# Performance work log

Hardware: AMD Instinct MI355X
Metric: run time of the kernel (lower is better)

Reference implementation:

```python
import jax, jax.numpy as jnp
import numpy as np

G = 7          # 7x7 feature map -> 49 nodes per image
N = G * G
K = 3          # knn_k
NEG_SLOPE = 0.2  # PyG GATConv default leaky_relu slope


def build_spatial_edges():
    # 8-neighborhood grid edges on the 7x7 map, directed (src -> dst)
    src, dst = [], []
    for r in range(G):
        for c in range(G):
            i = r * G + c
            for dr in (-1, 0, 1):
                for dc in (-1, 0, 1):
                    if dr == 0 and dc == 0:
                        continue
                    rr, cc = r + dr, c + dc
                    if 0 <= rr < G and 0 <= cc < G:
                        src.append(rr * G + cc)
                        dst.append(i)
    return np.array([src, dst], dtype=np.int32)

SPATIAL = build_spatial_edges()  # [2, 312]


def build_edges(x):
    """x: [B, N, F] node features -> (src, dst) each [B, E].
    Edges = spatial 8-neighborhood + feature-space kNN (k=3) + self-loops."""
    B = x.shape[0]
    sq = jnp.sum(x * x, axis=-1)                               # [B, N]
    d = sq[:, :, None] + sq[:, None, :] - 2.0 * jnp.einsum('bnf,bmf->bnm', x, x)
    d = d + jnp.eye(N, dtype=x.dtype) * 1e9                    # exclude self
    _, nbr = jax.lax.top_k(-d, K)                              # [B, N, K]
    knn_src = nbr.reshape(B, N * K)
    knn_dst = jnp.broadcast_to(jnp.repeat(jnp.arange(N, dtype=jnp.int32), K)[None], (B, N * K))
    sp = jnp.asarray(SPATIAL)
    Es = sp.shape[1]
    loops = jnp.arange(N, dtype=jnp.int32)
    src = jnp.concatenate([jnp.broadcast_to(sp[0][None], (B, Es)), knn_src.astype(jnp.int32),
                           jnp.broadcast_to(loops[None], (B, N))], axis=1)
    dst = jnp.concatenate([jnp.broadcast_to(sp[1][None], (B, Es)), knn_dst,
                           jnp.broadcast_to(loops[None], (B, N))], axis=1)
    return src, dst


def gat_layer(x, src, dst, W, a_src, a_dst, b, concat):
    """PyG-style GATConv (eval mode, no dropout). x: [N,F], src/dst: [E]."""
    H, C = a_src.shape
    h = (x @ W).reshape(N, H, C)                               # [N, H, C]
    es = jnp.sum(h * a_src[None], axis=-1)                     # [N, H]
    ed = jnp.sum(h * a_dst[None], axis=-1)                     # [N, H]
    e = jax.nn.leaky_relu(es[src] + ed[dst], NEG_SLOPE)        # [E, H]
    m = jax.ops.segment_max(e, dst, num_segments=N)            # [N, H]
    m = jnp.where(jnp.isfinite(m), m, 0.0)
    p = jnp.exp(e - m[dst])
    denom = jax.ops.segment_sum(p, dst, num_segments=N)
    alpha = p / jnp.maximum(denom[dst], 1e-16)                 # softmax over incoming edges
    out = jax.ops.segment_sum(alpha[:, :, None] * h[src], dst, num_segments=N)  # [N, H, C]
    out = out.reshape(N, H * C) if concat else out.mean(axis=1)
    return out + b


def setup_inputs() -> dict:
    key = jax.random.key(0)
    ks = jax.random.split(key, 14)
    B, F, Hd, Cd, O, NC = 256, 1024, 8, 128, 256, 14
    s = 0.05
    return {
        'feat_map': jax.random.normal(ks[0], (B, F, G, G), dtype=jnp.float32),
        'W1': jax.random.normal(ks[1], (F, Hd * Cd), dtype=jnp.float32) * s,
        'a_src1': jax.random.normal(ks[2], (Hd, Cd), dtype=jnp.float32) * s,
        'a_dst1': jax.random.normal(ks[3], (Hd, Cd), dtype=jnp.float32) * s,
        'b1': jnp.zeros((Hd * Cd,), dtype=jnp.float32),
        'W2': jax.random.normal(ks[4], (Hd * Cd, O), dtype=jnp.float32) * s,
        'a_src2': jax.random.normal(ks[5], (1, O), dtype=jnp.float32) * s,
        'a_dst2': jax.random.normal(ks[6], (1, O), dtype=jnp.float32) * s,
        'b2': jnp.zeros((O,), dtype=jnp.float32),
        'Wc1': jax.random.normal(ks[7], (O, O), dtype=jnp.float32) * s,
        'bc1': jnp.zeros((O,), dtype=jnp.float32),
        'Wc2': jax.random.normal(ks[8], (O, NC), dtype=jnp.float32) * s,
        'bc2': jnp.zeros((NC,), dtype=jnp.float32),
    }


def reference(feat_map, W1, a_src1, a_dst1, b1, W2, a_src2, a_dst2, b2, Wc1, bc1, Wc2, bc2):
    B = feat_map.shape[0]
    # backbone output relu + flatten 7x7 map into 49 nodes
    x = jax.nn.relu(feat_map).reshape(B, -1, N).transpose(0, 2, 1)  # [B, N, 1024]
    src, dst = build_edges(x)

    def per_graph(xg, sg, dg):
        h = jax.nn.elu(gat_layer(xg, sg, dg, W1, a_src1, a_dst1, b1, True))
        h = jax.nn.elu(gat_layer(h, sg, dg, W2, a_src2, a_dst2, b2, False))
        return h.mean(axis=0)                                   # global mean pool -> [256]

    pooled = jax.vmap(per_graph)(x, src, dst)                   # [B, 256]
    return jax.nn.relu(pooled @ Wc1 + bc1) @ Wc2 + bc2          # [B, 14]
```

## Files before the change

kernel.cpp:

```cpp
#include <hip/hip_runtime.h>

#define GDIM 7
#define NN 49
#define FDIM 1024
#define HD 8
#define CD 128
#define ODIM 256
#define NC 14
#define MAXE 12

typedef __attribute__((ext_vector_type(4))) float f32x4;
typedef __attribute__((ext_vector_type(8))) short s16x8;

struct us4 { unsigned short x, y, z, w; };

__device__ __forceinline__ unsigned short f2bf(float x) {
  unsigned u = __float_as_uint(x);
  return (unsigned short)((u + 0x7fffu + ((u >> 16) & 1u)) >> 16);
}
__device__ __forceinline__ float bf2f(unsigned short h) {
  return __uint_as_float((unsigned)h << 16);
}

#define GLOAD_LDS16(g, l)                                          \
  __builtin_amdgcn_global_load_lds(                                \
      (const __attribute__((address_space(1))) void*)(g),          \
      (__attribute__((address_space(3))) void*)(l), 16, 0, 0)

__global__ void __launch_bounds__(256) relu_transpose_kernel(
    const float* __restrict__ F, float* __restrict__ X,
    unsigned short* __restrict__ Xh, unsigned short* __restrict__ Xl) {
  const int b  = blockIdx.x >> 4;
  const int f0 = (blockIdx.x & 15) << 6;
  const int tid = threadIdx.x;
  __shared__ float lds[64 * NN];
  const float* src = F + (size_t)b * FDIM * NN + (size_t)f0 * NN;
  for (int idx = tid; idx < 64 * NN; idx += 256) lds[idx] = src[idx];
  __syncthreads();
  for (int pass = 0; pass < 13; pass++) {
    int n = pass * 4 + (tid >> 6);
    int fi = tid & 63;
    if (n < NN) {
      float v = lds[fi * NN + n];
      v = v > 0.f ? v : 0.f;
      size_t o = ((size_t)b * NN + n) * FDIM + f0 + fi;
      X[o] = v;
      unsigned short h = f2bf(v);
      Xh[o] = h;
      Xl[o] = f2bf(v - bf2f(h));
    }
  }
}

__global__ void __launch_bounds__(256) knn_kernel(
    const float* __restrict__ X, int* __restrict__ knn) {
  const int b = blockIdx.x, tid = threadIdx.x;
  __shared__ float xs[56][68];
  __shared__ float gram[56][57];
  const float* Xb = X + (size_t)b * NN * FDIM;

  const int tr = tid / 14, tc = tid % 14;
  float acc[4][4];
#pragma unroll
  for (int i = 0; i < 4; i++)
#pragma unroll
    for (int j = 0; j < 4; j++) acc[i][j] = 0.f;

  for (int c0 = 0; c0 < FDIM; c0 += 64) {
    __syncthreads();
    for (int idx = tid; idx < NN * 16; idx += 256) {
      int n = idx >> 4, q = idx & 15;
      *(float4*)&xs[n][q << 2] =
          *(const float4*)&Xb[(size_t)n * FDIM + c0 + (q << 2)];
    }
    __syncthreads();
    if (tid < 196) {
#pragma unroll
      for (int k4 = 0; k4 < 64; k4 += 4) {
        float4 a[4], bb[4];
#pragma unroll
        for (int i = 0; i < 4; i++) a[i]  = *(const float4*)&xs[tr + 14 * i][k4];
#pragma unroll
        for (int j = 0; j < 4; j++) bb[j] = *(const float4*)&xs[tc + 14 * j][k4];
#pragma unroll
        for (int i = 0; i < 4; i++)
#pragma unroll
          for (int j = 0; j < 4; j++)
            acc[i][j] += a[i].x * bb[j].x + a[i].y * bb[j].y +
                         a[i].z * bb[j].z + a[i].w * bb[j].w;
      }
    }
  }
  if (tid < 196) {
#pragma unroll
    for (int i = 0; i < 4; i++)
#pragma unroll
      for (int j = 0; j < 4; j++) gram[tr + 14 * i][tc + 14 * j] = acc[i][j];
  }
  __syncthreads();
  if (tid < NN) {
    const int n = tid;
    const float sqn = gram[n][n];
    float d0 = 1e30f, d1 = 1e30f, d2 = 1e30f;
    int i0 = 0, i1 = 0, i2 = 0;
    for (int m = 0; m < NN; m++) {
      if (m == n) continue;
      float d = sqn + gram[m][m] - 2.f * gram[n][m];
      if (d < d0)      { d2=d1; i2=i1; d1=d0; i1=i0; d0=d; i0=m; }
      else if (d < d1) { d2=d1; i2=i1; d1=d;  i1=m; }
      else if (d < d2) { d2=d;  i2=m; }
    }
    knn[((size_t)b * NN + n) * 3 + 0] = i0;
    knn[((size_t)b * NN + n) * 3 + 1] = i1;
    knn[((size_t)b * NN + n) * 3 + 2] = i2;
  }
}

__global__ void __launch_bounds__(256) wconvT_kernel(
    const float* __restrict__ W, int K, int N,
    unsigned short* __restrict__ WhT, unsigned short* __restrict__ WlT) {
  __shared__ float t[64][65];
  const int nbx = N >> 6;
  const int bx = blockIdx.x % nbx, by = blockIdx.x / nbx;
  const int r0 = by << 6, c0 = bx << 6;
  const int tid = threadIdx.x;
#pragma unroll
  for (int i = 0; i < 16; i++) {
    int r = i * 4 + (tid >> 6), c = tid & 63;
    t[r][c] = W[(size_t)(r0 + r) * N + c0 + c];
  }
  __syncthreads();
#pragma unroll
  for (int i = 0; i < 16; i++) {
    int n = i * 4 + (tid >> 6);
    int k = tid & 63;
    float x = t[k][n];
    unsigned short h = f2bf(x);
    size_t o = (size_t)(c0 + n) * K + r0 + k;
    WhT[o] = h;
    WlT[o] = f2bf(x - bf2f(h));
  }
}

__global__ void __launch_bounds__(256) gemm_bf16x3(
    const unsigned short* __restrict__ A_h, const unsigned short* __restrict__ A_l,
    const unsigned short* __restrict__ BT_h, const unsigned short* __restrict__ BT_l,
    float* __restrict__ C, int M, int N, int K) {
  __shared__ unsigned short sAh[128][64], sAl[128][64];
  __shared__ unsigned short sBh[128][64], sBl[128][64];
  const int tid = threadIdx.x;
  const int w = tid >> 6, lane = tid & 63;
  const int nbx = N >> 7;
  const int nwg = gridDim.x;
  const int q = nwg >> 3, r = nwg & 7;
  const int xcd = blockIdx.x & 7, loc = blockIdx.x >> 3;
  const int wg = (xcd < r) ? (xcd * (q + 1) + loc)
                           : (r * (q + 1) + (xcd - r) * q + loc);
  const int bx = wg % nbx, by = wg / nbx;
  const int row0 = by << 7, col0 = bx << 7;
  const int wr = (w >> 1) << 6, wc = (w & 1) << 6;
  const int sgr = lane >> 3;
  const int schunk = lane & 7;
  const int fr = lane & 15;
  const int fq = lane >> 4;

  f32x4 acc[4][4];
#pragma unroll
  for (int m = 0; m < 4; m++)
#pragma unroll
    for (int n = 0; n < 4; n++) acc[m][n] = (f32x4){0.f, 0.f, 0.f, 0.f};

  for (int k0 = 0; k0 < K; k0 += 64) {
    __syncthreads();
#pragma unroll
    for (int i = 0; i < 4; i++) {
      const int rbase = (w << 5) + (i << 3);
      const int gr = rbase + sgr;
      const int sc = schunk ^ (gr & 7);
      const size_t ga = (size_t)(row0 + gr) * K + k0 + (sc << 3);
      GLOAD_LDS16(A_h + ga, &sAh[rbase][0]);
      GLOAD_LDS16(A_l + ga, &sAl[rbase][0]);
      const size_t gb = (size_t)(col0 + gr) * K + k0 + (sc << 3);
      GLOAD_LDS16(BT_h + gb, &sBh[rbase][0]);
      GLOAD_LDS16(BT_l + gb, &sBl[rbase][0]);
    }
    __syncthreads();
#pragma unroll
    for (int ks = 0; ks < 2; ks++) {
      const int cb = (ks << 2) + fq;
      s16x8 ah[4], al[4], bh[4], bl[4];
#pragma unroll
      for (int m = 0; m < 4; m++) {
        const int ra = wr + (m << 4) + fr;
        const int ca = (cb ^ (ra & 7)) << 3;
        ah[m] = *(const s16x8*)&sAh[ra][ca];
        al[m] = *(const s16x8*)&sAl[ra][ca];
        const int rb = wc + (m << 4) + fr;
        const int cbn = (cb ^ (rb & 7)) << 3;
        bh[m] = *(const s16x8*)&sBh[rb][cbn];
        bl[m] = *(const s16x8*)&sBl[rb][cbn];
      }
#pragma unroll
      for (int m = 0; m < 4; m++)
#pragma unroll
        for (int n = 0; n < 4; n++) {
          acc[m][n] = __builtin_amdgcn_mfma_f32_16x16x32_bf16(ah[m], bh[n], acc[m][n], 0, 0, 0);
          acc[m][n] = __builtin_amdgcn_mfma_f32_16x16x32_bf16(ah[m], bl[n], acc[m][n], 0, 0, 0);
          acc[m][n] = __builtin_amdgcn_mfma_f32_16x16x32_bf16(al[m], bh[n], acc[m][n], 0, 0, 0);
        }
    }
  }
  const int crow = fq << 2, ccol = fr;
#pragma unroll
  for (int m = 0; m < 4; m++)
#pragma unroll
    for (int n = 0; n < 4; n++)
#pragma unroll
      for (int v = 0; v < 4; v++)
        C[(size_t)(row0 + wr + (m << 4) + crow + v) * N + col0 + wc + (n << 4) + ccol] =
            acc[m][n][v];
}

__global__ void __launch_bounds__(256) attn1_prep(
    const float* __restrict__ H, const int* __restrict__ knn,
    const float* __restrict__ a_src, const float* __restrict__ a_dst,
    int* __restrict__ srcs_g, int* __restrict__ cnt_g,
    float* __restrict__ alpha_g) {
  const int b = blockIdx.x, tid = threadIdx.x;
  __shared__ float es[NN][HD], ed[NN][HD];
  __shared__ int srcs[NN][MAXE];
  __shared__ int cnt[NN];
  const float* Hb = H + (size_t)b * NN * FDIM;

  for (int p = tid; p < NN * HD; p += 256) {
    int n = p >> 3, h = p & 7;
    const float* hr = Hb + (size_t)n * FDIM + h * CD;
    float s1 = 0.f, s2 = 0.f;
    for (int c = 0; c < CD; c += 4) {
      float4 hv = *(const float4*)&hr[c];
      float4 as = *(const float4*)&a_src[h * CD + c];
      float4 ad = *(const float4*)&a_dst[h * CD + c];
      s1 += hv.x*as.x + hv.y*as.y + hv.z*as.z + hv.w*as.w;
      s2 += hv.x*ad.x + hv.y*ad.y + hv.z*ad.z + hv.w*ad.w;
    }
    es[n][h] = s1; ed[n][h] = s2;
  }
  if (tid < NN) {
    int i = tid, r = i / GDIM, c = i % GDIM, k = 0;
    for (int dr = -1; dr <= 1; dr++)
      for (int dc = -1; dc <= 1; dc++) {
        if (dr == 0 && dc == 0) continue;
        int rr = r + dr, cc = c + dc;
        if (rr >= 0 && rr < GDIM && cc >= 0 && cc < GDIM)
          srcs[i][k++] = rr * GDIM + cc;
      }
    srcs[i][k++] = knn[((size_t)b * NN + i) * 3 + 0];
    srcs[i][k++] = knn[((size_t)b * NN + i) * 3 + 1];
    srcs[i][k++] = knn[((size_t)b * NN + i) * 3 + 2];
    srcs[i][k++] = i;
    cnt[i] = k;
    cnt_g[(size_t)b * NN + i] = k;
    for (int j = 0; j < MAXE; j++)
      srcs_g[((size_t)b * NN + i) * MAXE + j] = srcs[i][j < k ? j : 0];
  }
  __syncthreads();
  for (int p = tid; p < NN * HD; p += 256) {
    int i = p >> 3, h = p & 7;
    int k = cnt[i];
    float e[MAXE];
    float m = -1e30f;
#pragma unroll
    for (int j = 0; j < MAXE; j++) {
      if (j < k) {
        float v = es[srcs[i][j]][h] + ed[i][h];
        v = v >= 0.f ? v : 0.2f * v;
        e[j] = v;
        m = fmaxf(m, v);
      }
    }
    float denom = 0.f;
#pragma unroll
    for (int j = 0; j < MAXE; j++) {
      if (j < k) { e[j] = expf(e[j] - m); denom += e[j]; }
    }
    float inv = 1.f / fmaxf(denom, 1e-16f);
#pragma unroll
    for (int j = 0; j < MAXE; j++) {
      if (j < k)
        alpha_g[(((size_t)b * NN + i) * MAXE + j) * HD + h] = e[j] * inv;
    }
  }
}

__global__ void __launch_bounds__(256) attn1_agg(
    const float* __restrict__ H, const int* __restrict__ srcs_g,
    const int* __restrict__ cnt_g, const float* __restrict__ alpha_g,
    const float* __restrict__ b1,
    unsigned short* __restrict__ Zh, unsigned short* __restrict__ Zl) {
  const int bid = blockIdx.x;
  const int b = bid / NN;
  const int tid = threadIdx.x;
  __shared__ float al[MAXE][HD];
  __shared__ int ss[MAXE];
  const int k = cnt_g[bid];
  if (tid < MAXE * HD) al[tid >> 3][tid & 7] = alpha_g[(size_t)bid * MAXE * HD + tid];
  if (tid < MAXE) ss[tid] = srcs_g[(size_t)bid * MAXE + tid];
  __syncthreads();
  const float4* Hb = (const float4*)(H + (size_t)b * NN * FDIM);
  const int h = tid >> 5;
  float4 acc = ((const float4*)b1)[tid];
  for (int j = 0; j < k; j++) {
    float a = al[j][h];
    float4 v = Hb[(size_t)ss[j] * (FDIM / 4) + tid];
    acc.x += a * v.x; acc.y += a * v.y; acc.z += a * v.z; acc.w += a * v.w;
  }
  acc.x = acc.x > 0.f ? acc.x : expm1f(acc.x);
  acc.y = acc.y > 0.f ? acc.y : expm1f(acc.y);
  acc.z = acc.z > 0.f ? acc.z : expm1f(acc.z);
  acc.w = acc.w > 0.f ? acc.w : expm1f(acc.w);
  us4 hv, lv;
  hv.x = f2bf(acc.x); lv.x = f2bf(acc.x - bf2f(hv.x));
  hv.y = f2bf(acc.y); lv.y = f2bf(acc.y - bf2f(hv.y));
  hv.z = f2bf(acc.z); lv.z = f2bf(acc.z - bf2f(hv.z));
  hv.w = f2bf(acc.w); lv.w = f2bf(acc.w - bf2f(hv.w));
  *(us4*)&Zh[(size_t)bid * FDIM + (tid << 2)] = hv;
  *(us4*)&Zl[(size_t)bid * FDIM + (tid << 2)] = lv;
}

__global__ void __launch_bounds__(256) attn2_prep(
    const float* __restrict__ H2, const int* __restrict__ srcs_g,
    const int* __restrict__ cnt_g, const float* __restrict__ a_src,
    const float* __restrict__ a_dst, float* __restrict__ alpha_g) {
  const int b = blockIdx.x, tid = threadIdx.x;
  __shared__ float es[NN], ed[NN];
  const float* Hb = H2 + (size_t)b * NN * ODIM;
  if (tid < NN) {
    const float* hr = Hb + (size_t)tid * ODIM;
    float s1 = 0.f, s2 = 0.f;
    for (int c = 0; c < ODIM; c += 4) {
      float4 hv = *(const float4*)&hr[c];
      float4 as = *(const float4*)&a_src[c];
      float4 ad = *(const float4*)&a_dst[c];
      s1 += hv.x*as.x + hv.y*as.y + hv.z*as.z + hv.w*as.w;
      s2 += hv.x*ad.x + hv.y*ad.y + hv.z*ad.z + hv.w*ad.w;
    }
    es[tid] = s1; ed[tid] = s2;
  }
  __syncthreads();
  if (tid < NN) {
    const int i = tid;
    const int k = cnt_g[(size_t)b * NN + i];
    float e[MAXE];
    float m = -1e30f;
#pragma unroll
    for (int j = 0; j < MAXE; j++) {
      if (j < k) {
        int s = srcs_g[((size_t)b * NN + i) * MAXE + j];
        float v = es[s] + ed[i];
        v = v >= 0.f ? v : 0.2f * v;
        e[j] = v;
        m = fmaxf(m, v);
      }
    }
    float denom = 0.f;
#pragma unroll
    for (int j = 0; j < MAXE; j++) {
      if (j < k) { e[j] = expf(e[j] - m); denom += e[j]; }
    }
    float inv = 1.f / fmaxf(denom, 1e-16f);
#pragma unroll
    for (int j = 0; j < MAXE; j++) {
      if (j < k) alpha_g[((size_t)b * NN + i) * MAXE + j] = e[j] * inv;
    }
  }
}

__global__ void __launch_bounds__(256) attn2_agg(
    const float* __restrict__ H2, const int* __restrict__ srcs_g,
    const int* __restrict__ cnt_g, const float* __restrict__ alpha_g,
    const float* __restrict__ b2, float* __restrict__ Z2) {
  const int bid = blockIdx.x;
  const int b = bid / NN;
  const int tid = threadIdx.x;
  __shared__ float al[MAXE];
  __shared__ int ss[MAXE];
  const int k = cnt_g[bid];
  if (tid < MAXE) {
    al[tid] = alpha_g[(size_t)bid * MAXE + tid];
    ss[tid] = srcs_g[(size_t)bid * MAXE + tid];
  }
  __syncthreads();
  const float* Hb = H2 + (size_t)b * NN * ODIM;
  float acc = b2[tid];
  for (int j = 0; j < k; j++)
    acc += al[j] * Hb[(size_t)ss[j] * ODIM + tid];
  acc = acc > 0.f ? acc : expm1f(acc);
  Z2[(size_t)bid * ODIM + tid] = acc;
}

__global__ void __launch_bounds__(256) pool_kernel(
    const float* __restrict__ Z2, float* __restrict__ pooled) {
  const int b = blockIdx.x, c = threadIdx.x;
  float s = 0.f;
  for (int i = 0; i < NN; i++)
    s += Z2[((size_t)b * NN + i) * ODIM + c];
  pooled[(size_t)b * ODIM + c] = s * (1.f / 49.f);
}

__global__ void __launch_bounds__(256) classifier_kernel(
    const float* __restrict__ pooled, const float* __restrict__ Wc1,
    const float* __restrict__ bc1, const float* __restrict__ Wc2,
    const float* __restrict__ bc2, float* __restrict__ out) {
  const int b = blockIdx.x, tid = threadIdx.x;
  __shared__ float p[ODIM];
  __shared__ float t[ODIM];
  p[tid] = pooled[(size_t)b * ODIM + tid];
  __syncthreads();
  float a = bc1[tid];
  for (int c = 0; c < ODIM; c++) a += p[c] * Wc1[(size_t)c * ODIM + tid];
  t[tid] = a > 0.f ? a : 0.f;
  __syncthreads();
  if (tid < NC) {
    float o = bc2[tid];
    for (int j = 0; j < ODIM; j++) o += t[j] * Wc2[(size_t)j * NC + tid];
    out[(size_t)b * NC + tid] = o;
  }
}

extern "C" void kernel_launch(void* const* d_in, const int* in_sizes, int n_in,
                              void* d_out, int out_size, void* d_ws, size_t ws_size,
                              hipStream_t stream) {
  const float* feat   = (const float*)d_in[0];
  const float* W1     = (const float*)d_in[1];
  const float* a_src1 = (const float*)d_in[2];
  const float* a_dst1 = (const float*)d_in[3];
  const float* b1     = (const float*)d_in[4];
  const float* W2     = (const float*)d_in[5];
  const float* a_src2 = (const float*)d_in[6];
  const float* a_dst2 = (const float*)d_in[7];
  const float* b2     = (const float*)d_in[8];
  const float* Wc1    = (const float*)d_in[9];
  const float* bc1    = (const float*)d_in[10];
  const float* Wc2    = (const float*)d_in[11];
  const float* bc2    = (const float*)d_in[12];

  const int B = in_sizes[0] / (FDIM * NN);
  const int M = B * NN;

  const size_t xE = (size_t)M * FDIM;
  float* X  = (float*)d_ws;
  float* H1 = X + xE;
  unsigned short* Xh = (unsigned short*)(H1 + xE);
  unsigned short* Xl = Xh + xE;
  unsigned short* W1hT = Xl + xE;
  unsigned short* W1lT = W1hT + (size_t)FDIM * FDIM;
  unsigned short* W2hT = W1lT + (size_t)FDIM * FDIM;
  unsigned short* W2lT = W2hT + (size_t)ODIM * FDIM;
  int*   knn    = (int*)(W2lT + (size_t)ODIM * FDIM);
  int*   srcs_g = knn + (size_t)M * 3;
  int*   cnt_g  = srcs_g + (size_t)M * MAXE;
  float* alpha1 = (float*)(cnt_g + M);
  float* alpha2 = alpha1 + (size_t)M * MAXE * HD;
  float* pooled = alpha2 + (size_t)M * MAXE;
  float* H2  = X;
  float* Z2  = H1;
  unsigned short* Z1h = Xh;
  unsigned short* Z1l = Xl;

  relu_transpose_kernel<<<B * 16, 256, 0, stream>>>(feat, X, Xh, Xl);
  knn_kernel<<<B, 256, 0, stream>>>(X, knn);
  wconvT_kernel<<<(FDIM / 64) * (FDIM / 64), 256, 0, stream>>>(W1, FDIM, FDIM, W1hT, W1lT);
  wconvT_kernel<<<(FDIM / 64) * (ODIM / 64), 256, 0, stream>>>(W2, FDIM, ODIM, W2hT, W2lT);
  gemm_bf16x3<<<(M / 128) * (FDIM / 128), 256, 0, stream>>>(
      Xh, Xl, W1hT, W1lT, H1, M, FDIM, FDIM);
  attn1_prep<<<B, 256, 0, stream>>>(H1, knn, a_src1, a_dst1, srcs_g, cnt_g, alpha1);
  attn1_agg<<<M, 256, 0, stream>>>(H1, srcs_g, cnt_g, alpha1, b1, Z1h, Z1l);
  gemm_bf16x3<<<(M / 128) * (ODIM / 128), 256, 0, stream>>>(
      Z1h, Z1l, W2hT, W2lT, H2, M, ODIM, FDIM);
  attn2_prep<<<B, 256, 0, stream>>>(H2, srcs_g, cnt_g, a_src2, a_dst2, alpha2);
  attn2_agg<<<M, 256, 0, stream>>>(H2, srcs_g, cnt_g, alpha2, b2, Z2);
  pool_kernel<<<B, 256, 0, stream>>>(Z2, pooled);
  classifier_kernel<<<B, 256, 0, stream>>>(pooled, Wc1, bc1, Wc2, bc2, (float*)d_out);
}
```

Measured before the change: 325.2 us.

## Split kNN gram and attention score kernels across more blocks; fuse pooling

```diff
diff --git a/kernel.cpp b/kernel.cpp
--- a/kernel.cpp
+++ b/kernel.cpp
@@ -8,6 +8,8 @@
 #define ODIM 256
 #define NC 14
 #define MAXE 12
+#define KSPLIT 4
+#define GPSTRIDE 3192
 
 typedef __attribute__((ext_vector_type(4))) float f32x4;
 typedef __attribute__((ext_vector_type(8))) short s16x8;
@@ -52,12 +54,13 @@
   }
 }
 
-__global__ void __launch_bounds__(256) knn_kernel(
-    const float* __restrict__ X, int* __restrict__ knn) {
-  const int b = blockIdx.x, tid = threadIdx.x;
+__global__ void __launch_bounds__(256) knn_partial(
+    const float* __restrict__ X, float* __restrict__ gramP) {
+  const int gid = blockIdx.x;
+  const int b = gid >> 2, p = gid & 3;
+  const int tid = threadIdx.x;
   __shared__ float xs[56][68];
-  __shared__ float gram[56][57];
-  const float* Xb = X + (size_t)b * NN * FDIM;
+  const float* Xb = X + (size_t)b * NN * FDIM + p * 256;
 
   const int tr = tid / 14, tc = tid % 14;
   float acc[4][4];
@@ -66,7 +69,7 @@
 #pragma unroll
     for (int j = 0; j < 4; j++) acc[i][j] = 0.f;
 
-  for (int c0 = 0; c0 < FDIM; c0 += 64) {
+  for (int c0 = 0; c0 < 256; c0 += 64) {
     __syncthreads();
     for (int idx = tid; idx < NN * 16; idx += 256) {
       int n = idx >> 4, q = idx & 15;
@@ -92,10 +95,25 @@
     }
   }
   if (tid < 196) {
+    float* gp = gramP + (size_t)gid * GPSTRIDE;
 #pragma unroll
     for (int i = 0; i < 4; i++)
 #pragma unroll
-      for (int j = 0; j < 4; j++) gram[tr + 14 * i][tc + 14 * j] = acc[i][j];
+      for (int j = 0; j < 4; j++)
+        gp[(tr + 14 * i) * 57 + tc + 14 * j] = acc[i][j];
+  }
+}
+
+__global__ void __launch_bounds__(256) knn_select(
+    const float* __restrict__ gramP, int* __restrict__ knn) {
+  const int b = blockIdx.x, tid = threadIdx.x;
+  __shared__ float gram[NN][50];
+  const float* g0 = gramP + (size_t)(b * KSPLIT) * GPSTRIDE;
+  for (int idx = tid; idx < NN * NN; idx += 256) {
+    int r = idx / NN, c = idx % NN;
+    float s = g0[r * 57 + c] + g0[GPSTRIDE + r * 57 + c] +
+              g0[2 * GPSTRIDE + r * 57 + c] + g0[3 * GPSTRIDE + r * 57 + c];
+    gram[r][c] = s;
   }
   __syncthreads();
   if (tid < NN) {
@@ -221,29 +239,44 @@
             acc[m][n][v];
 }
 
-__global__ void __launch_bounds__(256) attn1_prep(
-    const float* __restrict__ H, const int* __restrict__ knn,
-    const float* __restrict__ a_src, const float* __restrict__ a_dst,
-    int* __restrict__ srcs_g, int* __restrict__ cnt_g,
-    float* __restrict__ alpha_g) {
+__global__ void __launch_bounds__(256) esed1_kernel(
+    const float* __restrict__ H, const float* __restrict__ a_src,
+    const float* __restrict__ a_dst, float* __restrict__ es_g,
+    float* __restrict__ ed_g) {
+  const int n = blockIdx.x * 4 + (threadIdx.x >> 6);
+  const int lane = threadIdx.x & 63;
+  const int h = lane >> 3, sub = lane & 7;
+  const float* hr = H + (size_t)n * FDIM + h * CD + sub * 16;
+  const float* as = a_src + h * CD + sub * 16;
+  const float* ad = a_dst + h * CD + sub * 16;
+  float s1 = 0.f, s2 = 0.f;
+#pragma unroll
+  for (int c = 0; c < 16; c += 4) {
+    float4 hv = *(const float4*)&hr[c];
+    float4 av = *(const float4*)&as[c];
+    float4 dv = *(const float4*)&ad[c];
+    s1 += hv.x*av.x + hv.y*av.y + hv.z*av.z + hv.w*av.w;
+    s2 += hv.x*dv.x + hv.y*dv.y + hv.z*dv.z + hv.w*dv.w;
+  }
+  s1 += __shfl_xor(s1, 1); s1 += __shfl_xor(s1, 2); s1 += __shfl_xor(s1, 4);
+  s2 += __shfl_xor(s2, 1); s2 += __shfl_xor(s2, 2); s2 += __shfl_xor(s2, 4);
+  if (sub == 0) {
+    es_g[(size_t)n * HD + h] = s1;
+    ed_g[(size_t)n * HD + h] = s2;
+  }
+}
+
+__global__ void __launch_bounds__(256) attn1_soft(
+    const float* __restrict__ es_g, const float* __restrict__ ed_g,
+    const int* __restrict__ knn, int* __restrict__ srcs_g,
+    int* __restrict__ cnt_g, float* __restrict__ alpha_g) {
   const int b = blockIdx.x, tid = threadIdx.x;
   __shared__ float es[NN][HD], ed[NN][HD];
   __shared__ int srcs[NN][MAXE];
   __shared__ int cnt[NN];
-  const float* Hb = H + (size_t)b * NN * FDIM;
-
   for (int p = tid; p < NN * HD; p += 256) {
-    int n = p >> 3, h = p & 7;
-    const float* hr = Hb + (size_t)n * FDIM + h * CD;
-    float s1 = 0.f, s2 = 0.f;
-    for (int c = 0; c < CD; c += 4) {
-      float4 hv = *(const float4*)&hr[c];
-      float4 as = *(const float4*)&a_src[h * CD + c];
-      float4 ad = *(const float4*)&a_dst[h * CD + c];
-      s1 += hv.x*as.x + hv.y*as.y + hv.z*as.z + hv.w*as.w;
-      s2 += hv.x*ad.x + hv.y*ad.y + hv.z*ad.z + hv.w*ad.w;
-    }
-    es[n][h] = s1; ed[n][h] = s2;
+    es[p >> 3][p & 7] = es_g[(size_t)b * NN * HD + p];
+    ed[p >> 3][p & 7] = ed_g[(size_t)b * NN * HD + p];
   }
   if (tid < NN) {
     int i = tid, r = i / GDIM, c = i % GDIM, k = 0;
@@ -327,24 +360,34 @@
   *(us4*)&Zl[(size_t)bid * FDIM + (tid << 2)] = lv;
 }
 
-__global__ void __launch_bounds__(256) attn2_prep(
-    const float* __restrict__ H2, const int* __restrict__ srcs_g,
-    const int* __restrict__ cnt_g, const float* __restrict__ a_src,
-    const float* __restrict__ a_dst, float* __restrict__ alpha_g) {
+__global__ void __launch_bounds__(256) esed2_kernel(
+    const float* __restrict__ H2, const float* __restrict__ a_src,
+    const float* __restrict__ a_dst, float* __restrict__ es_g,
+    float* __restrict__ ed_g) {
+  const int n = blockIdx.x * 4 + (threadIdx.x >> 6);
+  const int lane = threadIdx.x & 63;
+  float4 hv = *(const float4*)&H2[(size_t)n * ODIM + lane * 4];
+  float4 av = *(const float4*)&a_src[lane * 4];
+  float4 dv = *(const float4*)&a_dst[lane * 4];
+  float s1 = hv.x*av.x + hv.y*av.y + hv.z*av.z + hv.w*av.w;
+  float s2 = hv.x*dv.x + hv.y*dv.y + hv.z*dv.z + hv.w*dv.w;
+#pragma unroll
+  for (int m = 1; m < 64; m <<= 1) {
+    s1 += __shfl_xor(s1, m);
+    s2 += __shfl_xor(s2, m);
+  }
+  if (lane == 0) { es_g[n] = s1; ed_g[n] = s2; }
+}
+
+__global__ void __launch_bounds__(256) attn2_soft(
+    const float* __restrict__ es_g, const float* __restrict__ ed_g,
+    const int* __restrict__ srcs_g, const int* __restrict__ cnt_g,
+    float* __restrict__ alpha_g) {
   const int b = blockIdx.x, tid = threadIdx.x;
   __shared__ float es[NN], ed[NN];
-  const float* Hb = H2 + (size_t)b * NN * ODIM;
   if (tid < NN) {
-    const float* hr = Hb + (size_t)tid * ODIM;
-    float s1 = 0.f, s2 = 0.f;
-    for (int c = 0; c < ODIM; c += 4) {
-      float4 hv = *(const float4*)&hr[c];
-      float4 as = *(const float4*)&a_src[c];
-      float4 ad = *(const float4*)&a_dst[c];
-      s1 += hv.x*as.x + hv.y*as.y + hv.z*as.z + hv.w*as.w;
-      s2 += hv.x*ad.x + hv.y*ad.y + hv.z*ad.z + hv.w*ad.w;
-    }
-    es[tid] = s1; ed[tid] = s2;
+    es[tid] = es_g[(size_t)b * NN + tid];
+    ed[tid] = ed_g[(size_t)b * NN + tid];
   }
   __syncthreads();
   if (tid < NN) {
@@ -398,23 +441,17 @@
   Z2[(size_t)bid * ODIM + tid] = acc;
 }
 
-__global__ void __launch_bounds__(256) pool_kernel(
-    const float* __restrict__ Z2, float* __restrict__ pooled) {
-  const int b = blockIdx.x, c = threadIdx.x;
-  float s = 0.f;
-  for (int i = 0; i < NN; i++)
-    s += Z2[((size_t)b * NN + i) * ODIM + c];
-  pooled[(size_t)b * ODIM + c] = s * (1.f / 49.f);
-}
-
 __global__ void __launch_bounds__(256) classifier_kernel(
-    const float* __restrict__ pooled, const float* __restrict__ Wc1,
+    const float* __restrict__ Z2, const float* __restrict__ Wc1,
     const float* __restrict__ bc1, const float* __restrict__ Wc2,
     const float* __restrict__ bc2, float* __restrict__ out) {
   const int b = blockIdx.x, tid = threadIdx.x;
   __shared__ float p[ODIM];
   __shared__ float t[ODIM];
-  p[tid] = pooled[(size_t)b * ODIM + tid];
+  float s = 0.f;
+  for (int i = 0; i < NN; i++)
+    s += Z2[((size_t)b * NN + i) * ODIM + tid];
+  p[tid] = s * (1.f / 49.f);
   __syncthreads();
   float a = bc1[tid];
   for (int c = 0; c < ODIM; c++) a += p[c] * Wc1[(size_t)c * ODIM + tid];
@@ -461,24 +498,30 @@
   int*   cnt_g  = srcs_g + (size_t)M * MAXE;
   float* alpha1 = (float*)(cnt_g + M);
   float* alpha2 = alpha1 + (size_t)M * MAXE * HD;
-  float* pooled = alpha2 + (size_t)M * MAXE;
+  float* gramP  = alpha2 + (size_t)M * MAXE;
+  float* es1    = gramP + (size_t)B * KSPLIT * GPSTRIDE;
+  float* ed1    = es1 + (size_t)M * HD;
+  float* es2    = ed1 + (size_t)M * HD;
+  float* ed2    = es2 + M;
   float* H2  = X;
   float* Z2  = H1;
   unsigned short* Z1h = Xh;
   unsigned short* Z1l = Xl;
 
   relu_transpose_kernel<<<B * 16, 256, 0, stream>>>(feat, X, Xh, Xl);
-  knn_kernel<<<B, 256, 0, stream>>>(X, knn);
+  knn_partial<<<B * KSPLIT, 256, 0, stream>>>(X, gramP);
+  knn_select<<<B, 256, 0, stream>>>(gramP, knn);
   wconvT_kernel<<<(FDIM / 64) * (FDIM / 64), 256, 0, stream>>>(W1, FDIM, FDIM, W1hT, W1lT);
   wconvT_kernel<<<(FDIM / 64) * (ODIM / 64), 256, 0, stream>>>(W2, FDIM, ODIM, W2hT, W2lT);
   gemm_bf16x3<<<(M / 128) * (FDIM / 128), 256, 0, stream>>>(
       Xh, Xl, W1hT, W1lT, H1, M, FDIM, FDIM);
-  attn1_prep<<<B, 256, 0, stream>>>(H1, knn, a_src1, a_dst1, srcs_g, cnt_g, alpha1);
+  esed1_kernel<<<M / 4, 256, 0, stream>>>(H1, a_src1, a_dst1, es1, ed1);
+  attn1_soft<<<B, 256, 0, stream>>>(es1, ed1, knn, srcs_g, cnt_g, alpha1);
   attn1_agg<<<M, 256, 0, stream>>>(H1, srcs_g, cnt_g, alpha1, b1, Z1h, Z1l);
   gemm_bf16x3<<<(M / 128) * (ODIM / 128), 256, 0, stream>>>(
       Z1h, Z1l, W2hT, W2lT, H2, M, ODIM, FDIM);
-  attn2_prep<<<B, 256, 0, stream>>>(H2, srcs_g, cnt_g, a_src2, a_dst2, alpha2);
+  esed2_kernel<<<M / 4, 256, 0, stream>>>(H2, a_src2, a_dst2, es2, ed2);
+  attn2_soft<<<B, 256, 0, stream>>>(es2, ed2, srcs_g, cnt_g, alpha2);
   attn2_agg<<<M, 256, 0, stream>>>(H2, srcs_g, cnt_g, alpha2, b2, Z2);
-  pool_kernel<<<B, 256, 0, stream>>>(Z2, pooled);
-  classifier_kernel<<<B, 256, 0, stream>>>(pooled, Wc1, bc1, Wc2, bc2, (float*)d_out);
-}
+  classifier_kernel<<<B, 256, 0, stream>>>(Z2, Wc1, bc1, Wc2, bc2, (float*)d_out);
+}
```

Result: no change. 328.9 us (+1.2%).

## Fuse attention logits into GEMM epilogues and drop prep and pool kernels

Applied to the files above, without the earlier changes.

```diff
diff --git a/kernel.cpp b/kernel.cpp
--- a/kernel.cpp
+++ b/kernel.cpp
@@ -53,7 +53,8 @@
 }
 
 __global__ void __launch_bounds__(256) knn_kernel(
-    const float* __restrict__ X, int* __restrict__ knn) {
+    const float* __restrict__ X, int* __restrict__ srcs_g,
+    int* __restrict__ cnt_g) {
   const int b = blockIdx.x, tid = threadIdx.x;
   __shared__ float xs[56][68];
   __shared__ float gram[56][57];
@@ -110,9 +111,20 @@
       else if (d < d1) { d2=d1; i2=i1; d1=d;  i1=m; }
       else if (d < d2) { d2=d;  i2=m; }
     }
-    knn[((size_t)b * NN + n) * 3 + 0] = i0;
-    knn[((size_t)b * NN + n) * 3 + 1] = i1;
-    knn[((size_t)b * NN + n) * 3 + 2] = i2;
+    int srcs[MAXE];
+    int r = n / GDIM, c = n % GDIM, k = 0;
+    for (int dr = -1; dr <= 1; dr++)
+      for (int dc = -1; dc <= 1; dc++) {
+        if (dr == 0 && dc == 0) continue;
+        int rr = r + dr, cc = c + dc;
+        if (rr >= 0 && rr < GDIM && cc >= 0 && cc < GDIM)
+          srcs[k++] = rr * GDIM + cc;
+      }
+    srcs[k++] = i0; srcs[k++] = i1; srcs[k++] = i2;
+    srcs[k++] = n;
+    cnt_g[(size_t)b * NN + n] = k;
+    for (int j = 0; j < MAXE; j++)
+      srcs_g[((size_t)b * NN + n) * MAXE + j] = srcs[j < k ? j : 0];
   }
 }
 
@@ -145,7 +157,9 @@
 __global__ void __launch_bounds__(256) gemm_bf16x3(
     const unsigned short* __restrict__ A_h, const unsigned short* __restrict__ A_l,
     const unsigned short* __restrict__ BT_h, const unsigned short* __restrict__ BT_l,
-    float* __restrict__ C, int M, int N, int K) {
+    float* __restrict__ C, int M, int N, int K,
+    const float* __restrict__ av, const float* __restrict__ dv,
+    float* __restrict__ esp, float* __restrict__ edp) {
   __shared__ unsigned short sAh[128][64], sAl[128][64];
   __shared__ unsigned short sBh[128][64], sBl[128][64];
   const int tid = threadIdx.x;
@@ -219,92 +233,86 @@
       for (int v = 0; v < 4; v++)
         C[(size_t)(row0 + wr + (m << 4) + crow + v) * N + col0 + wc + (n << 4) + ccol] =
             acc[m][n][v];
-}
-
-__global__ void __launch_bounds__(256) attn1_prep(
-    const float* __restrict__ H, const int* __restrict__ knn,
-    const float* __restrict__ a_src, const float* __restrict__ a_dst,
-    int* __restrict__ srcs_g, int* __restrict__ cnt_g,
-    float* __restrict__ alpha_g) {
-  const int b = blockIdx.x, tid = threadIdx.x;
-  __shared__ float es[NN][HD], ed[NN][HD];
-  __shared__ int srcs[NN][MAXE];
-  __shared__ int cnt[NN];
-  const float* Hb = H + (size_t)b * NN * FDIM;
-
-  for (int p = tid; p < NN * HD; p += 256) {
-    int n = p >> 3, h = p & 7;
-    const float* hr = Hb + (size_t)n * FDIM + h * CD;
-    float s1 = 0.f, s2 = 0.f;
-    for (int c = 0; c < CD; c += 4) {
-      float4 hv = *(const float4*)&hr[c];
-      float4 as = *(const float4*)&a_src[h * CD + c];
-      float4 ad = *(const float4*)&a_dst[h * CD + c];
-      s1 += hv.x*as.x + hv.y*as.y + hv.z*as.z + hv.w*as.w;
-      s2 += hv.x*ad.x + hv.y*ad.y + hv.z*ad.z + hv.w*ad.w;
-    }
-    es[n][h] = s1; ed[n][h] = s2;
-  }
-  if (tid < NN) {
-    int i = tid, r = i / GDIM, c = i % GDIM, k = 0;
-    for (int dr = -1; dr <= 1; dr++)
-      for (int dc = -1; dc <= 1; dc++) {
-        if (dr == 0 && dc == 0) continue;
-        int rr = r + dr, cc = c + dc;
-        if (rr >= 0 && rr < GDIM && cc >= 0 && cc < GDIM)
-          srcs[i][k++] = rr * GDIM + cc;
-      }
-    srcs[i][k++] = knn[((size_t)b * NN + i) * 3 + 0];
-    srcs[i][k++] = knn[((size_t)b * NN + i) * 3 + 1];
-    srcs[i][k++] = knn[((size_t)b * NN + i) * 3 + 2];
-    srcs[i][k++] = i;
-    cnt[i] = k;
-    cnt_g[(size_t)b * NN + i] = k;
-    for (int j = 0; j < MAXE; j++)
-      srcs_g[((size_t)b * NN + i) * MAXE + j] = srcs[i][j < k ? j : 0];
-  }
-  __syncthreads();
-  for (int p = tid; p < NN * HD; p += 256) {
-    int i = p >> 3, h = p & 7;
-    int k = cnt[i];
-    float e[MAXE];
-    float m = -1e30f;
-#pragma unroll
-    for (int j = 0; j < MAXE; j++) {
-      if (j < k) {
-        float v = es[srcs[i][j]][h] + ed[i][h];
-        v = v >= 0.f ? v : 0.2f * v;
-        e[j] = v;
-        m = fmaxf(m, v);
-      }
-    }
-    float denom = 0.f;
-#pragma unroll
-    for (int j = 0; j < MAXE; j++) {
-      if (j < k) { e[j] = expf(e[j] - m); denom += e[j]; }
-    }
-    float inv = 1.f / fmaxf(denom, 1e-16f);
-#pragma unroll
-    for (int j = 0; j < MAXE; j++) {
-      if (j < k)
-        alpha_g[(((size_t)b * NN + i) * MAXE + j) * HD + h] = e[j] * inv;
-    }
-  }
+
+  const int pstride = N >> 6;
+  const int part = (col0 + wc) >> 6;
+  float asv[4], adv[4];
+#pragma unroll
+  for (int n = 0; n < 4; n++) {
+    int cidx = col0 + wc + (n << 4) + fr;
+    asv[n] = av[cidx];
+    adv[n] = dv[cidx];
+  }
+#pragma unroll
+  for (int m = 0; m < 4; m++)
+#pragma unroll
+    for (int v = 0; v < 4; v++) {
+      float s = acc[m][0][v] * asv[0] + acc[m][1][v] * asv[1] +
+                acc[m][2][v] * asv[2] + acc[m][3][v] * asv[3];
+      float d = acc[m][0][v] * adv[0] + acc[m][1][v] * adv[1] +
+                acc[m][2][v] * adv[2] + acc[m][3][v] * adv[3];
+      s += __shfl_xor(s, 1); s += __shfl_xor(s, 2);
+      s += __shfl_xor(s, 4); s += __shfl_xor(s, 8);
+      d += __shfl_xor(d, 1); d += __shfl_xor(d, 2);
+      d += __shfl_xor(d, 4); d += __shfl_xor(d, 8);
+      if (fr == 0) {
+        int row = row0 + wr + (m << 4) + (fq << 2) + v;
+        esp[(size_t)row * pstride + part] = s;
+        edp[(size_t)row * pstride + part] = d;
+      }
+    }
 }
 
 __global__ void __launch_bounds__(256) attn1_agg(
     const float* __restrict__ H, const int* __restrict__ srcs_g,
-    const int* __restrict__ cnt_g, const float* __restrict__ alpha_g,
-    const float* __restrict__ b1,
+    const int* __restrict__ cnt_g, const float* __restrict__ es1p,
+    const float* __restrict__ ed1p, const float* __restrict__ b1,
     unsigned short* __restrict__ Zh, unsigned short* __restrict__ Zl) {
   const int bid = blockIdx.x;
   const int b = bid / NN;
   const int tid = threadIdx.x;
+  __shared__ int ss[MAXE];
+  __shared__ float se[MAXE][HD];
+  __shared__ float edv[HD];
   __shared__ float al[MAXE][HD];
-  __shared__ int ss[MAXE];
   const int k = cnt_g[bid];
-  if (tid < MAXE * HD) al[tid >> 3][tid & 7] = alpha_g[(size_t)bid * MAXE * HD + tid];
   if (tid < MAXE) ss[tid] = srcs_g[(size_t)bid * MAXE + tid];
+  __syncthreads();
+  if (tid < MAXE * HD) {
+    int j = tid >> 3, h = tid & 7;
+    size_t base = ((size_t)b * NN + ss[j]) * 16 + h * 2;
+    se[j][h] = es1p[base] + es1p[base + 1];
+  }
+  if (tid >= 128 && tid < 128 + HD) {
+    int h = tid - 128;
+    size_t base = (size_t)bid * 16 + h * 2;
+    edv[h] = ed1p[base] + ed1p[base + 1];
+  }
+  __syncthreads();
+  if (tid < HD) {
+    const int h = tid;
+    float e[MAXE];
+    float m = -1e30f;
+#pragma unroll
+    for (int j = 0; j < MAXE; j++) {
+      if (j < k) {
+        float v = se[j][h] + edv[h];
+        v = v >= 0.f ? v : 0.2f * v;
+        e[j] = v;
+        m = fmaxf(m, v);
+      }
+    }
+    float denom = 0.f;
+#pragma unroll
+    for (int j = 0; j < MAXE; j++) {
+      if (j < k) { e[j] = expf(e[j] - m); denom += e[j]; }
+    }
+    float inv = 1.f / fmaxf(denom, 1e-16f);
+#pragma unroll
+    for (int j = 0; j < MAXE; j++) {
+      if (j < k) al[j][h] = e[j] * inv;
+    }
+  }
   __syncthreads();
   const float4* Hb = (const float4*)(H + (size_t)b * NN * FDIM);
   const int h = tid >> 5;
@@ -327,36 +335,34 @@
   *(us4*)&Zl[(size_t)bid * FDIM + (tid << 2)] = lv;
 }
 
-__global__ void __launch_bounds__(256) attn2_prep(
+__global__ void __launch_bounds__(256) attn2_agg(
     const float* __restrict__ H2, const int* __restrict__ srcs_g,
-    const int* __restrict__ cnt_g, const float* __restrict__ a_src,
-    const float* __restrict__ a_dst, float* __restrict__ alpha_g) {
-  const int b = blockIdx.x, tid = threadIdx.x;
-  __shared__ float es[NN], ed[NN];
-  const float* Hb = H2 + (size_t)b * NN * ODIM;
-  if (tid < NN) {
-    const float* hr = Hb + (size_t)tid * ODIM;
-    float s1 = 0.f, s2 = 0.f;
-    for (int c = 0; c < ODIM; c += 4) {
-      float4 hv = *(const float4*)&hr[c];
-      float4 as = *(const float4*)&a_src[c];
-      float4 ad = *(const float4*)&a_dst[c];
-      s1 += hv.x*as.x + hv.y*as.y + hv.z*as.z + hv.w*as.w;
-      s2 += hv.x*ad.x + hv.y*ad.y + hv.z*ad.z + hv.w*ad.w;
-    }
-    es[tid] = s1; ed[tid] = s2;
-  }
-  __syncthreads();
-  if (tid < NN) {
-    const int i = tid;
-    const int k = cnt_g[(size_t)b * NN + i];
+    const int* __restrict__ cnt_g, const float* __restrict__ es2p,
+    const float* __restrict__ ed2p, const float* __restrict__ b2,
+    float* __restrict__ Z2) {
+  const int bid = blockIdx.x;
+  const int b = bid / NN;
+  const int tid = threadIdx.x;
+  __shared__ int ss[MAXE];
+  __shared__ float se[MAXE];
+  __shared__ float al[MAXE];
+  const int k = cnt_g[bid];
+  if (tid < MAXE) ss[tid] = srcs_g[(size_t)bid * MAXE + tid];
+  __syncthreads();
+  if (tid < MAXE) {
+    size_t base = ((size_t)b * NN + ss[tid]) * 4;
+    se[tid] = es2p[base] + es2p[base + 1] + es2p[base + 2] + es2p[base + 3];
+  }
+  __syncthreads();
+  if (tid == 0) {
+    size_t base = (size_t)bid * 4;
+    float ed = ed2p[base] + ed2p[base + 1] + ed2p[base + 2] + ed2p[base + 3];
     float e[MAXE];
     float m = -1e30f;
 #pragma unroll
     for (int j = 0; j < MAXE; j++) {
       if (j < k) {
-        int s = srcs_g[((size_t)b * NN + i) * MAXE + j];
-        float v = es[s] + ed[i];
+        float v = se[j] + ed;
         v = v >= 0.f ? v : 0.2f * v;
         e[j] = v;
         m = fmaxf(m, v);
@@ -370,24 +376,8 @@
     float inv = 1.f / fmaxf(denom, 1e-16f);
 #pragma unroll
     for (int j = 0; j < MAXE; j++) {
-      if (j < k) alpha_g[((size_t)b * NN + i) * MAXE + j] = e[j] * inv;
-    }
-  }
-}
-
-__global__ void __launch_bounds__(256) attn2_agg(
-    const float* __restrict__ H2, const int* __restrict__ srcs_g,
-    const int* __restrict__ cnt_g, const float* __restrict__ alpha_g,
-    const float* __restrict__ b2, float* __restrict__ Z2) {
-  const int bid = blockIdx.x;
-  const int b = bid / NN;
-  const int tid = threadIdx.x;
-  __shared__ float al[MAXE];
-  __shared__ int ss[MAXE];
-  const int k = cnt_g[bid];
-  if (tid < MAXE) {
-    al[tid] = alpha_g[(size_t)bid * MAXE + tid];
-    ss[tid] = srcs_g[(size_t)bid * MAXE + tid];
+      if (j < k) al[j] = e[j] * inv;
+    }
   }
   __syncthreads();
   const float* Hb = H2 + (size_t)b * NN * ODIM;
@@ -398,23 +388,17 @@
   Z2[(size_t)bid * ODIM + tid] = acc;
 }
 
-__global__ void __launch_bounds__(256) pool_kernel(
-    const float* __restrict__ Z2, float* __restrict__ pooled) {
-  const int b = blockIdx.x, c = threadIdx.x;
-  float s = 0.f;
-  for (int i = 0; i < NN; i++)
-    s += Z2[((size_t)b * NN + i) * ODIM + c];
-  pooled[(size_t)b * ODIM + c] = s * (1.f / 49.f);
-}
-
 __global__ void __launch_bounds__(256) classifier_kernel(
-    const float* __restrict__ pooled, const float* __restrict__ Wc1,
+    const float* __restrict__ Z2, const float* __restrict__ Wc1,
     const float* __restrict__ bc1, const float* __restrict__ Wc2,
     const float* __restrict__ bc2, float* __restrict__ out) {
   const int b = blockIdx.x, tid = threadIdx.x;
   __shared__ float p[ODIM];
   __shared__ float t[ODIM];
-  p[tid] = pooled[(size_t)b * ODIM + tid];
+  float s = 0.f;
+  for (int i = 0; i < NN; i++)
+    s += Z2[((size_t)b * NN + i) * ODIM + tid];
+  p[tid] = s * (1.f / 49.f);
   __syncthreads();
   float a = bc1[tid];
   for (int c = 0; c < ODIM; c++) a += p[c] * Wc1[(size_t)c * ODIM + tid];
@@ -456,29 +440,26 @@
   unsigned short* W1lT = W1hT + (size_t)FDIM * FDIM;
   unsigned short* W2hT = W1lT + (size_t)FDIM * FDIM;
   unsigned short* W2lT = W2hT + (size_t)ODIM * FDIM;
-  int*   knn    = (int*)(W2lT + (size_t)ODIM * FDIM);
-  int*   srcs_g = knn + (size_t)M * 3;
+  int*   srcs_g = (int*)(W2lT + (size_t)ODIM * FDIM);
   int*   cnt_g  = srcs_g + (size_t)M * MAXE;
-  float* alpha1 = (float*)(cnt_g + M);
-  float* alpha2 = alpha1 + (size_t)M * MAXE * HD;
-  float* pooled = alpha2 + (size_t)M * MAXE;
+  float* es1p   = (float*)(cnt_g + M);
+  float* ed1p   = es1p + (size_t)M * 16;
+  float* es2p   = ed1p + (size_t)M * 16;
+  float* ed2p   = es2p + (size_t)M * 4;
   float* H2  = X;
   float* Z2  = H1;
   unsigned short* Z1h = Xh;
   unsigned short* Z1l = Xl;
 
   relu_transpose_kernel<<<B * 16, 256, 0, stream>>>(feat, X, Xh, Xl);
-  knn_kernel<<<B, 256, 0, stream>>>(X, knn);
+  knn_kernel<<<B, 256, 0, stream>>>(X, srcs_g, cnt_g);
   wconvT_kernel<<<(FDIM / 64) * (FDIM / 64), 256, 0, stream>>>(W1, FDIM, FDIM, W1hT, W1lT);
   wconvT_kernel<<<(FDIM / 64) * (ODIM / 64), 256, 0, stream>>>(W2, FDIM, ODIM, W2hT, W2lT);
   gemm_bf16x3<<<(M / 128) * (FDIM / 128), 256, 0, stream>>>(
-      Xh, Xl, W1hT, W1lT, H1, M, FDIM, FDIM);
-  attn1_prep<<<B, 256, 0, stream>>>(H1, knn, a_src1, a_dst1, srcs_g, cnt_g, alpha1);
-  attn1_agg<<<M, 256, 0, stream>>>(H1, srcs_g, cnt_g, alpha1, b1, Z1h, Z1l);
+      Xh, Xl, W1hT, W1lT, H1, M, FDIM, FDIM, a_src1, a_dst1, es1p, ed1p);
+  attn1_agg<<<M, 256, 0, stream>>>(H1, srcs_g, cnt_g, es1p, ed1p, b1, Z1h, Z1l);
   gemm_bf16x3<<<(M / 128) * (ODIM / 128), 256, 0, stream>>>(
-      Z1h, Z1l, W2hT, W2lT, H2, M, ODIM, FDIM);
-  attn2_prep<<<B, 256, 0, stream>>>(H2, srcs_g, cnt_g, a_src2, a_dst2, alpha2);
-  attn2_agg<<<M, 256, 0, stream>>>(H2, srcs_g, cnt_g, alpha2, b2, Z2);
-  pool_kernel<<<B, 256, 0, stream>>>(Z2, pooled);
-  classifier_kernel<<<B, 256, 0, stream>>>(pooled, Wc1, bc1, Wc2, bc2, (float*)d_out);
-}
+      Z1h, Z1l, W2hT, W2lT, H2, M, ODIM, FDIM, a_src2, a_dst2, es2p, ed2p);
+  attn2_agg<<<M, 256, 0, stream>>>(H2, srcs_g, cnt_g, es2p, ed2p, b2, Z2);
+  classifier_kernel<<<B, 256, 0, stream>>>(Z2, Wc1, bc1, Wc2, bc2, (float*)d_out);
+}
```

After: 314.9 us. -3.2%, faster.
